# Optimization experiments

Hardware: AMD Instinct MI355X
Metric: run time of the kernel (lower is better)

The kernel has to match this reference:

```python
import jax, jax.numpy as jnp
import numpy as np

N = 50000   # nodes
E = 400000  # edges
IN_DIM, H1, H2, OUT_DIM = 512, 256, 62, 128


def _param(key, shape, scale=0.05):
    return jax.random.normal(key, shape, dtype=jnp.float32) * scale


def setup_inputs() -> dict:
    key = jax.random.key(0)
    ks = jax.random.split(key, 24)
    x = jax.random.normal(ks[0], (N, IN_DIM), dtype=jnp.float32)
    edge_index_neg = jax.random.randint(ks[1], (2, E), 0, N, dtype=jnp.int64)
    d = {
        "x": x, "edge_index_neg": edge_index_neg,
        # nn.Linear params (W stored as [in, out])
        "W1": _param(ks[2], (IN_DIM, H1)), "b1": _param(ks[3], (H1,)),
        "W2": _param(ks[4], (H1, H2)),    "b2": _param(ks[5], (H2,)),
        "W3": _param(ks[6], (H2, OUT_DIM)), "b3": _param(ks[7], (OUT_DIM,)),
        # GCNConv params: lin weight (no bias) + post-aggregation bias
        "Wg1": _param(ks[8], (H1, H1)),   "bg1": _param(ks[9], (H1,)),
        "Wg2": _param(ks[10], (H2, H2)),  "bg2": _param(ks[11], (H2,)),
        "Wg3": _param(ks[12], (OUT_DIM, OUT_DIM)), "bg3": _param(ks[13], (OUT_DIM,)),
        "Wg4": _param(ks[14], (OUT_DIM, OUT_DIM)), "bg4": _param(ks[15], (OUT_DIM,)),
        "Wg5": _param(ks[16], (OUT_DIM, OUT_DIM)), "bg5": _param(ks[17], (OUT_DIM,)),
        "Wg6": _param(ks[18], (OUT_DIM, OUT_DIM)), "bg6": _param(ks[19], (OUT_DIM,)),
    }
    return d


def _build_norm(edge_index):
    # PyG GCNConv: add self-loops, symmetric normalization D^-1/2 A D^-1/2
    loop = jnp.arange(N, dtype=edge_index.dtype)
    src = jnp.concatenate([edge_index[0], loop])
    dst = jnp.concatenate([edge_index[1], loop])
    deg = jax.ops.segment_sum(jnp.ones_like(dst, dtype=jnp.float32), dst, num_segments=N)
    dinv = jnp.where(deg > 0, jax.lax.rsqrt(jnp.maximum(deg, 1.0)), 0.0)
    norm = dinv[src] * dinv[dst]  # [E+N]
    return src, dst, norm


def _gcn(x, W, b, src, dst, norm):
    h = x @ W                                   # [N, F]
    msg = h[src] * norm[:, None]                # gather + edge scale
    out = jax.ops.segment_sum(msg, dst, num_segments=N)  # scatter-add
    return out + b


def reference(x, edge_index_neg, W1, b1, W2, b2, W3, b3,
              Wg1, bg1, Wg2, bg2, Wg3, bg3, Wg4, bg4, Wg5, bg5, Wg6, bg6):
    src, dst, norm = _build_norm(edge_index_neg)
    relu = jax.nn.relu
    x1l = x @ W1 + b1
    x1 = x1l + relu(_gcn(x1l, Wg1, bg1, src, dst, norm))
    x2l = x1 @ W2 + b2
    x2 = x2l + relu(_gcn(x2l, Wg2, bg2, src, dst, norm))
    x3l = x2 @ W3 + b3
    x3 = x3l + 0.5 * relu(_gcn(x3l, Wg3, bg3, src, dst, norm))
    x4 = x3 + 0.5 * relu(_gcn(x4_in := x3, Wg4, bg4, src, dst, norm))
    x5 = x4 + 0.25 * relu(_gcn(x4, Wg5, bg5, src, dst, norm))
    x6 = x5 + 0.25 * _gcn(x5, Wg6, bg6, src, dst, norm)
    return x6
```

## Files before the change

### kernel.cpp

```cpp
#include <hip/hip_runtime.h>

#define NN 50000
#define NE 400000
#define NBLK 196

using short8 = __attribute__((ext_vector_type(8))) short;
using f32x4  = __attribute__((ext_vector_type(4))) float;
using f32x2  = __attribute__((ext_vector_type(2))) float;
using u16x2  = __attribute__((ext_vector_type(2))) unsigned short;
using u16x4  = __attribute__((ext_vector_type(4))) unsigned short;

__device__ __forceinline__ unsigned short f2b(float f) {
    union { float f; unsigned int u; } x; x.f = f;
    unsigned int u = x.u;
    u += 0x7fffu + ((u >> 16) & 1u);
    return (unsigned short)(u >> 16);
}
__device__ __forceinline__ float b2f(unsigned short u) {
    union { unsigned int u; float f; } x; x.u = ((unsigned int)u) << 16;
    return x.f;
}

#define SWZ(b, row) ((b) ^ (((row) & 7) << 4))

__device__ __forceinline__ void gload16(const void* g, void* l) {
    __builtin_amdgcn_global_load_lds(
        (const __attribute__((address_space(1))) void*)g,
        (__attribute__((address_space(3))) void*)l, 16, 0, 0);
}

__global__ __launch_bounds__(256) void zero2_k(int* a, int* b) {
    int i = blockIdx.x * 256 + threadIdx.x;
    if (i < NN) { a[i] = 0; b[i] = 0; }
}
__global__ __launch_bounds__(256) void count_k(const int* __restrict__ dst, int* __restrict__ indeg) {
    int e = blockIdx.x * 256 + threadIdx.x;
    if (e < NE) atomicAdd(&indeg[dst[e]], 1);
}
__global__ __launch_bounds__(256) void scan1_k(const int* __restrict__ indeg, int* __restrict__ tmp,
                                               int* __restrict__ bsum) {
    __shared__ int s[256];
    int t = threadIdx.x, i = blockIdx.x * 256 + t;
    int v = (i < NN) ? indeg[i] : 0;
    s[t] = v; __syncthreads();
    for (int off = 1; off < 256; off <<= 1) {
        int x = (t >= off) ? s[t - off] : 0;
        __syncthreads();
        s[t] += x;
        __syncthreads();
    }
    if (i < NN) tmp[i] = s[t];
    if (t == 255) bsum[blockIdx.x] = s[255];
}
__global__ __launch_bounds__(256) void scan2_k(const int* __restrict__ bsum, int* __restrict__ boff) {
    __shared__ int s[256];
    int t = threadIdx.x;
    int v = (t < NBLK) ? bsum[t] : 0;
    s[t] = v; __syncthreads();
    for (int off = 1; off < 256; off <<= 1) {
        int x = (t >= off) ? s[t - off] : 0;
        __syncthreads();
        s[t] += x;
        __syncthreads();
    }
    if (t < NBLK) boff[t] = s[t] - v;
}
__global__ __launch_bounds__(256) void scan3_k(const int* __restrict__ tmp, const int* __restrict__ indeg,
                                               const int* __restrict__ boff, int* __restrict__ rowptr,
                                               float* __restrict__ dinv) {
    int i = blockIdx.x * 256 + threadIdx.x;
    if (i < NN) {
        rowptr[i] = tmp[i] - indeg[i] + boff[i >> 8];
        dinv[i] = rsqrtf((float)(1 + indeg[i]));
    }
    if (i == 0) rowptr[NN] = NE;
}
__global__ __launch_bounds__(256) void fill_k(const int* __restrict__ src, const int* __restrict__ dst,
                                              const float* __restrict__ dinv, const int* __restrict__ rowptr,
                                              int* __restrict__ cursor, int2* __restrict__ ebn) {
    int e = blockIdx.x * 256 + threadIdx.x;
    if (e >= NE) return;
    int s = src[e], d = dst[e];
    int pos = atomicAdd(&cursor[d], 1);
    ebn[rowptr[d] + pos] = make_int2(s, __float_as_int(dinv[s] * dinv[d]));
}

__global__ __launch_bounds__(256) void xcast_k(const float* __restrict__ x, unsigned short* __restrict__ xb) {
    long i = (long)blockIdx.x * 256 + threadIdx.x;
    const long total = (long)NN * 512 / 8;
    if (i >= total) return;
    float4 f0 = *(const float4*)(x + i * 8);
    float4 f1 = *(const float4*)(x + i * 8 + 4);
    short8 v;
    v[0] = (short)f2b(f0.x); v[1] = (short)f2b(f0.y);
    v[2] = (short)f2b(f0.z); v[3] = (short)f2b(f0.w);
    v[4] = (short)f2b(f1.x); v[5] = (short)f2b(f1.y);
    v[6] = (short)f2b(f1.z); v[7] = (short)f2b(f1.w);
    *(short8*)(xb + i * 8) = v;
}

struct WSegs {
    const float* W[9];
    unsigned short* Wt[9];
    int K[9], N[9], Kp[9];
    int c0[10];
};
__global__ __launch_bounds__(256) void wcast_all_k(WSegs s) {
    int blk = blockIdx.x;
    #pragma unroll
    for (int g = 0; g < 9; g++) {
        if (blk >= s.c0[g] && blk < s.c0[g + 1]) {
            int idx = (blk - s.c0[g]) * 256 + threadIdx.x;
            int Kp = s.Kp[g];
            int n = idx / Kp, k = idx % Kp;
            float v = (n < s.N[g] && k < s.K[g]) ? s.W[g][(size_t)k * s.N[g] + n] : 0.0f;
            s.Wt[g][idx] = f2b(v);
        }
    }
}

template<int BM, int BN>
__global__ __launch_bounds__(256) void gemm_mfma_k(
    const unsigned short* __restrict__ A, const unsigned short* __restrict__ Bt,
    const float* __restrict__ bias, unsigned short* __restrict__ C,
    int M, int lda, int Kp, int N, int ldc) {
    constexpr int MR = BM / 32;
    constexpr int NF = BN / 32;
    constexpr int nA = BM / 32;
    constexpr int nB = BN / 32;
    constexpr int BUFB = (BM + BN) * 128;
    __shared__ __align__(16) char lds[2 * BUFB];

    int tid = threadIdx.x;
    int lane = tid & 63, wave = tid >> 6;
    int wr = wave >> 1, wc = wave & 1;
    int lr = lane & 15, lk = lane >> 4;
    int r0 = blockIdx.x * BM, c0 = blockIdx.y * BN;

    f32x4 acc[MR][NF];
    #pragma unroll
    for (int m = 0; m < MR; m++)
        #pragma unroll
        for (int n = 0; n < NF; n++)
            acc[m][n] = (f32x4){0.f, 0.f, 0.f, 0.f};

    auto ISSUE = [&](int k0, char* buf) {
        char* AsB = buf;
        char* BsB = buf + BM * 128;
        #pragma unroll
        for (int c = 0; c < nA; c++) {
            int o = tid + c * 256;
            int row = o >> 3;
            int octg = (o & 7) ^ (row & 7);
            int gr = min(r0 + row, M - 1);
            gload16(A + (size_t)gr * lda + k0 + octg * 8, AsB + o * 16);
        }
        #pragma unroll
        for (int c = 0; c < nB; c++) {
            int o = tid + c * 256;
            int row = o >> 3;
            int octg = (o & 7) ^ (row & 7);
            gload16(Bt + (size_t)(c0 + row) * Kp + k0 + octg * 8, BsB + o * 16);
        }
    };

    int nt = Kp >> 6;
    ISSUE(0, lds);
    __syncthreads();
    for (int t = 0; t < nt; t++) {
        char* cur = lds + (t & 1) * BUFB;
        if (t + 1 < nt) ISSUE((t + 1) << 6, lds + ((t + 1) & 1) * BUFB);
        char* AsB = cur;
        char* BsB = cur + BM * 128;
        #pragma unroll
        for (int kk = 0; kk < 2; kk++) {
            int kb = kk * 64 + lk * 16;
            short8 a[MR], b[NF];
            #pragma unroll
            for (int m = 0; m < MR; m++) {
                int row = wr * (BM / 2) + m * 16 + lr;
                a[m] = *(short8*)(AsB + SWZ(row * 128 + kb, row));
            }
            #pragma unroll
            for (int n = 0; n < NF; n++) {
                int row = wc * (BN / 2) + n * 16 + lr;
                b[n] = *(short8*)(BsB + SWZ(row * 128 + kb, row));
            }
            #pragma unroll
            for (int m = 0; m < MR; m++)
                #pragma unroll
                for (int n = 0; n < NF; n++)
                    acc[m][n] = __builtin_amdgcn_mfma_f32_16x16x32_bf16(a[m], b[n], acc[m][n], 0, 0, 0);
        }
        __syncthreads();
    }

    constexpr int LDC = BN + 8;
    unsigned short* ldsC = (unsigned short*)lds;
    #pragma unroll
    for (int n = 0; n < NF; n++) {
        int cc = wc * (BN / 2) + n * 16 + lr;
        int gc = c0 + cc;
        float bv = (bias != nullptr && gc < N) ? bias[gc] : 0.0f;
        bool ok = gc < N;
        #pragma unroll
        for (int m = 0; m < MR; m++)
            #pragma unroll
            for (int j = 0; j < 4; j++) {
                int row = wr * (BM / 2) + m * 16 + lk * 4 + j;
                float v = ok ? acc[m][n][j] + bv : 0.0f;
                ldsC[row * LDC + cc] = f2b(v);
            }
    }
    __syncthreads();
    constexpr int CH = (BM * BN) / 2048;
    #pragma unroll
    for (int c = 0; c < CH; c++) {
        int o = tid + c * 256;
        int row = o / (BN / 8), col = (o % (BN / 8)) * 8;
        int gr = r0 + row;
        if (gr < M)
            *(short8*)(C + (size_t)gr * ldc + c0 + col) = *(short8*)(ldsC + row * LDC + col);
    }
}

template<int VEC> struct BV;
template<> struct BV<1> { using T = unsigned short; };
template<> struct BV<2> { using T = u16x2; };
template<> struct BV<4> { using T = u16x4; };
template<int VEC> struct FV;
template<> struct FV<1> { using T = float; };
template<> struct FV<2> { using T = f32x2; };
template<> struct FV<4> { using T = f32x4; };

template<int VEC, int SPLIT, bool OUTF32>
__global__ __launch_bounds__(256) void gather_k(
    const unsigned short* __restrict__ h, const unsigned short* __restrict__ base,
    const float* __restrict__ dinv, const float* __restrict__ bias,
    const int2* __restrict__ ebn, const int* __restrict__ rowptr,
    void* __restrict__ outraw, float alpha, int dorelu, int F) {
    constexpr int ld = 64 * VEC * SPLIT;
    int gw = (blockIdx.x * 256 + threadIdx.x) >> 6;
    int lane = threadIdx.x & 63;
    int w = gw / SPLIT;
    int colbase = (gw % SPLIT) * 64 * VEC;
    if (w >= NN) return;
    using LT = typename BV<VEC>::T;
    const int col = colbase + lane * VEC;

    float acc[VEC];
    float dn = dinv[w];
    {
        LT t = *(const LT*)(h + (size_t)w * ld + col);
        const unsigned short* tu = (const unsigned short*)&t;
        #pragma unroll
        for (int v = 0; v < VEC; v++) acc[v] = b2f(tu[v]) * dn * dn;
    }
    int e = rowptr[w], end = rowptr[w + 1];
    for (; e + 8 <= end; e += 8) {
        long long q[8];
        #pragma unroll
        for (int i = 0; i < 8; i++)
            q[i] = __builtin_nontemporal_load((const long long*)(ebn + e + i));
        LT t[8];
        #pragma unroll
        for (int i = 0; i < 8; i++)
            t[i] = *(const LT*)(h + (size_t)(int)q[i] * ld + col);
        #pragma unroll
        for (int i = 0; i < 8; i++) {
            float nr = __int_as_float((int)(q[i] >> 32));
            const unsigned short* u = (const unsigned short*)&t[i];
            #pragma unroll
            for (int v = 0; v < VEC; v++) acc[v] += b2f(u[v]) * nr;
        }
    }
    for (; e + 2 <= end; e += 2) {
        long long q0 = __builtin_nontemporal_load((const long long*)(ebn + e));
        long long q1 = __builtin_nontemporal_load((const long long*)(ebn + e + 1));
        LT t0 = *(const LT*)(h + (size_t)(int)q0 * ld + col);
        LT t1 = *(const LT*)(h + (size_t)(int)q1 * ld + col);
        float n0 = __int_as_float((int)(q0 >> 32)), n1 = __int_as_float((int)(q1 >> 32));
        const unsigned short* u0 = (const unsigned short*)&t0;
        const unsigned short* u1 = (const unsigned short*)&t1;
        #pragma unroll
        for (int v = 0; v < VEC; v++) acc[v] += b2f(u0[v]) * n0 + b2f(u1[v]) * n1;
    }
    if (e < end) {
        long long q0 = __builtin_nontemporal_load((const long long*)(ebn + e));
        LT t0 = *(const LT*)(h + (size_t)(int)q0 * ld + col);
        float n0 = __int_as_float((int)(q0 >> 32));
        const unsigned short* u0 = (const unsigned short*)&t0;
        #pragma unroll
        for (int v = 0; v < VEC; v++) acc[v] += b2f(u0[v]) * n0;
    }
    LT bt = __builtin_nontemporal_load((const LT*)(base + (size_t)w * ld + col));
    const unsigned short* bu = (const unsigned short*)&bt;
    if (OUTF32) {
        typename FV<VEC>::T ot;
        float* of = (float*)&ot;
        #pragma unroll
        for (int v = 0; v < VEC; v++) {
            int f = col + v;
            float a = acc[v] + ((f < F) ? bias[f] : 0.0f);
            if (dorelu) a = fmaxf(a, 0.0f);
            of[v] = (f < F) ? b2f(bu[v]) + alpha * a : 0.0f;
        }
        __builtin_nontemporal_store(ot, (typename FV<VEC>::T*)((float*)outraw + (size_t)w * ld + col));
    } else {
        LT ot;
        unsigned short* ou = (unsigned short*)&ot;
        #pragma unroll
        for (int v = 0; v < VEC; v++) {
            int f = col + v;
            float a = acc[v] + ((f < F) ? bias[f] : 0.0f);
            if (dorelu) a = fmaxf(a, 0.0f);
            float res = (f < F) ? b2f(bu[v]) + alpha * a : 0.0f;
            ou[v] = f2b(res);
        }
        __builtin_nontemporal_store(ot, (LT*)((unsigned short*)outraw + (size_t)w * ld + col));
    }
}

extern "C" void kernel_launch(void* const* d_in, const int* in_sizes, int n_in,
                              void* d_out, int out_size, void* d_ws, size_t ws_size,
                              hipStream_t stream) {
    const float* x   = (const float*)d_in[0];
    const int*   ei  = (const int*)d_in[1];
    const float* W1  = (const float*)d_in[2];  const float* b1  = (const float*)d_in[3];
    const float* W2  = (const float*)d_in[4];  const float* b2  = (const float*)d_in[5];
    const float* W3  = (const float*)d_in[6];  const float* b3  = (const float*)d_in[7];
    const float* Wg1 = (const float*)d_in[8];  const float* bg1 = (const float*)d_in[9];
    const float* Wg2 = (const float*)d_in[10]; const float* bg2 = (const float*)d_in[11];
    const float* Wg3 = (const float*)d_in[12]; const float* bg3 = (const float*)d_in[13];
    const float* Wg4 = (const float*)d_in[14]; const float* bg4 = (const float*)d_in[15];
    const float* Wg5 = (const float*)d_in[16]; const float* bg5 = (const float*)d_in[17];
    const float* Wg6 = (const float*)d_in[18]; const float* bg6 = (const float*)d_in[19];
    const int* srcv = ei;
    const int* dstv = ei + NE;

    float* dinv = (float*)d_ws;
    unsigned short* xb = (unsigned short*)(dinv + 51200);
    unsigned short* hA = xb + (size_t)NN * 512;
    unsigned short* hB = hA + (size_t)NN * 256;
    unsigned short* hC = hB + (size_t)NN * 256;
    unsigned short* W1t  = hC + (size_t)NN * 256;
    unsigned short* Wg1t = W1t  + 256 * 512;
    unsigned short* W2t  = Wg1t + 256 * 256;
    unsigned short* Wg2t = W2t  + 64 * 256;
    unsigned short* W3t  = Wg2t + 64 * 64;
    unsigned short* Wg3t = W3t  + 128 * 64;
    unsigned short* Wg4t = Wg3t + 128 * 128;
    unsigned short* Wg5t = Wg4t + 128 * 128;
    unsigned short* Wg6t = Wg5t + 128 * 128;
    int* indeg  = (int*)(Wg6t + 128 * 128);
    int* cursor = indeg + 51200;
    int* tmp    = cursor + 51200;
    int* rowptr = tmp + 51200;
    int* bsum   = rowptr + 51264;
    int* boff   = bsum + 256;
    int2* ebn   = (int2*)(boff + 256);

    zero2_k<<<NBLK, 256, 0, stream>>>(indeg, cursor);
    count_k<<<(NE + 255) / 256, 256, 0, stream>>>(dstv, indeg);
    scan1_k<<<NBLK, 256, 0, stream>>>(indeg, tmp, bsum);
    scan2_k<<<1, 256, 0, stream>>>(bsum, boff);
    scan3_k<<<NBLK, 256, 0, stream>>>(tmp, indeg, boff, rowptr, dinv);
    fill_k<<<(NE + 255) / 256, 256, 0, stream>>>(srcv, dstv, dinv, rowptr, cursor, ebn);

    xcast_k<<<(int)(((long)NN * 512 / 8 + 255) / 256), 256, 0, stream>>>(x, xb);

    {
        WSegs s;
        const float* Ws[9] = {W1, Wg1, W2, Wg2, W3, Wg3, Wg4, Wg5, Wg6};
        unsigned short* Wts[9] = {W1t, Wg1t, W2t, Wg2t, W3t, Wg3t, Wg4t, Wg5t, Wg6t};
        int Ks[9]  = {512, 256, 256, 62, 62, 128, 128, 128, 128};
        int Ns[9]  = {256, 256, 62, 62, 128, 128, 128, 128, 128};
        int Kps[9] = {512, 256, 256, 64, 64, 128, 128, 128, 128};
        int Nps[9] = {256, 256, 64, 64, 128, 128, 128, 128, 128};
        int c = 0;
        for (int g = 0; g < 9; g++) {
            s.W[g] = Ws[g]; s.Wt[g] = Wts[g];
            s.K[g] = Ks[g]; s.N[g] = Ns[g]; s.Kp[g] = Kps[g];
            s.c0[g] = c;
            c += (Kps[g] * Nps[g]) / 256;
        }
        s.c0[9] = c;
        wcast_all_k<<<c, 256, 0, stream>>>(s);
    }

    const int GX = (NN + 63) / 64;
    const int GG1 = (NN * 64 + 255) / 256;
    const int GG2 = (NN * 2 * 64 + 255) / 256;

    gemm_mfma_k<64, 128><<<dim3(GX, 2), 256, 0, stream>>>(xb, W1t, b1, hA, NN, 512, 512, 256, 256);
    gemm_mfma_k<64, 128><<<dim3(GX, 2), 256, 0, stream>>>(hA, Wg1t, nullptr, hB, NN, 256, 256, 256, 256);
    gather_k<2, 2, false><<<GG2, 256, 0, stream>>>(hB, hA, dinv, bg1, ebn, rowptr, hC, 1.0f, 1, 256);
    gemm_mfma_k<64, 64><<<dim3(GX, 1), 256, 0, stream>>>(hC, W2t, b2, hA, NN, 256, 256, 62, 64);
    gemm_mfma_k<64, 64><<<dim3(GX, 1), 256, 0, stream>>>(hA, Wg2t, nullptr, hB, NN, 64, 64, 62, 64);
    gather_k<1, 1, false><<<GG1, 256, 0, stream>>>(hB, hA, dinv, bg2, ebn, rowptr, hC, 1.0f, 1, 62);
    gemm_mfma_k<64, 64><<<dim3(GX, 2), 256, 0, stream>>>(hC, W3t, b3, hA, NN, 64, 64, 128, 128);
    gemm_mfma_k<64, 64><<<dim3(GX, 2), 256, 0, stream>>>(hA, Wg3t, nullptr, hB, NN, 128, 128, 128, 128);
    gather_k<2, 1, false><<<GG1, 256, 0, stream>>>(hB, hA, dinv, bg3, ebn, rowptr, hC, 0.5f, 1, 128);
    gemm_mfma_k<64, 64><<<dim3(GX, 2), 256, 0, stream>>>(hC, Wg4t, nullptr, hA, NN, 128, 128, 128, 128);
    gather_k<2, 1, false><<<GG1, 256, 0, stream>>>(hA, hC, dinv, bg4, ebn, rowptr, hB, 0.5f, 1, 128);
    gemm_mfma_k<64, 64><<<dim3(GX, 2), 256, 0, stream>>>(hB, Wg5t, nullptr, hA, NN, 128, 128, 128, 128);
    gather_k<2, 1, false><<<GG1, 256, 0, stream>>>(hA, hB, dinv, bg5, ebn, rowptr, hC, 0.25f, 1, 128);
    gemm_mfma_k<64, 64><<<dim3(GX, 2), 256, 0, stream>>>(hC, Wg6t, nullptr, hA, NN, 128, 128, 128, 128);
    gather_k<2, 1, true><<<GG1, 256, 0, stream>>>(hA, hC, dinv, bg6, ebn, rowptr, d_out, 0.25f, 0, 128);
}
```

Before: 407.6 us.

## Process two destination nodes per wave in gather and widen GEMM N tiles

```diff
diff --git a/kernel.cpp b/kernel.cpp
--- a/kernel.cpp
+++ b/kernel.cpp
@@ -240,84 +240,143 @@
     const int2* __restrict__ ebn, const int* __restrict__ rowptr,
     void* __restrict__ outraw, float alpha, int dorelu, int F) {
     constexpr int ld = 64 * VEC * SPLIT;
+    using LT = typename BV<VEC>::T;
     int gw = (blockIdx.x * 256 + threadIdx.x) >> 6;
     int lane = threadIdx.x & 63;
-    int w = gw / SPLIT;
-    int colbase = (gw % SPLIT) * 64 * VEC;
-    if (w >= NN) return;
-    using LT = typename BV<VEC>::T;
-    const int col = colbase + lane * VEC;
-
-    float acc[VEC];
-    float dn = dinv[w];
+    int pair = gw / SPLIT;
+    int colseg = gw % SPLIT;
+    int w0 = pair * 2, w1 = w0 + 1;
+    if (w0 >= NN) return;
+    bool has1 = (w1 < NN);
+    const int col = colseg * 64 * VEC + lane * VEC;
+
+    float acc0[VEC], acc1[VEC];
+    float dn0 = dinv[w0];
     {
-        LT t = *(const LT*)(h + (size_t)w * ld + col);
+        LT t = *(const LT*)(h + (size_t)w0 * ld + col);
         const unsigned short* tu = (const unsigned short*)&t;
         #pragma unroll
-        for (int v = 0; v < VEC; v++) acc[v] = b2f(tu[v]) * dn * dn;
-    }
-    int e = rowptr[w], end = rowptr[w + 1];
-    for (; e + 8 <= end; e += 8) {
-        long long q[8];
-        #pragma unroll
-        for (int i = 0; i < 8; i++)
-            q[i] = __builtin_nontemporal_load((const long long*)(ebn + e + i));
-        LT t[8];
-        #pragma unroll
-        for (int i = 0; i < 8; i++)
-            t[i] = *(const LT*)(h + (size_t)(int)q[i] * ld + col);
-        #pragma unroll
-        for (int i = 0; i < 8; i++) {
+        for (int v = 0; v < VEC; v++) acc0[v] = b2f(tu[v]) * dn0 * dn0;
+    }
+    if (has1) {
+        float dn1 = dinv[w1];
+        LT t = *(const LT*)(h + (size_t)w1 * ld + col);
+        const unsigned short* tu = (const unsigned short*)&t;
+        #pragma unroll
+        for (int v = 0; v < VEC; v++) acc1[v] = b2f(tu[v]) * dn1 * dn1;
+    } else {
+        #pragma unroll
+        for (int v = 0; v < VEC; v++) acc1[v] = 0.0f;
+    }
+
+    int e0 = rowptr[w0], end0 = rowptr[w0 + 1];
+    int e1 = has1 ? end0 : 0, end1 = has1 ? rowptr[w1 + 1] : 0;
+
+    while (e0 + 4 <= end0 && e1 + 4 <= end1) {
+        long long q0[4], q1[4];
+        #pragma unroll
+        for (int i = 0; i < 4; i++) {
+            q0[i] = __builtin_nontemporal_load((const long long*)(ebn + e0 + i));
+            q1[i] = __builtin_nontemporal_load((const long long*)(ebn + e1 + i));
+        }
+        LT t0[4], t1[4];
+        #pragma unroll
+        for (int i = 0; i < 4; i++) {
+            t0[i] = *(const LT*)(h + (size_t)(int)q0[i] * ld + col);
+            t1[i] = *(const LT*)(h + (size_t)(int)q1[i] * ld + col);
+        }
+        #pragma unroll
+        for (int i = 0; i < 4; i++) {
+            float n0 = __int_as_float((int)(q0[i] >> 32));
+            float n1 = __int_as_float((int)(q1[i] >> 32));
+            const unsigned short* u0 = (const unsigned short*)&t0[i];
+            const unsigned short* u1 = (const unsigned short*)&t1[i];
+            #pragma unroll
+            for (int v = 0; v < VEC; v++) {
+                acc0[v] += b2f(u0[v]) * n0;
+                acc1[v] += b2f(u1[v]) * n1;
+            }
+        }
+        e0 += 4; e1 += 4;
+    }
+    for (; e0 + 4 <= end0; e0 += 4) {
+        long long q[4];
+        #pragma unroll
+        for (int i = 0; i < 4; i++) q[i] = __builtin_nontemporal_load((const long long*)(ebn + e0 + i));
+        LT t[4];
+        #pragma unroll
+        for (int i = 0; i < 4; i++) t[i] = *(const LT*)(h + (size_t)(int)q[i] * ld + col);
+        #pragma unroll
+        for (int i = 0; i < 4; i++) {
             float nr = __int_as_float((int)(q[i] >> 32));
             const unsigned short* u = (const unsigned short*)&t[i];
             #pragma unroll
-            for (int v = 0; v < VEC; v++) acc[v] += b2f(u[v]) * nr;
-        }
-    }
-    for (; e + 2 <= end; e += 2) {
-        long long q0 = __builtin_nontemporal_load((const long long*)(ebn + e));
-        long long q1 = __builtin_nontemporal_load((const long long*)(ebn + e + 1));
-        LT t0 = *(const LT*)(h + (size_t)(int)q0 * ld + col);
-        LT t1 = *(const LT*)(h + (size_t)(int)q1 * ld + col);
-        float n0 = __int_as_float((int)(q0 >> 32)), n1 = __int_as_float((int)(q1 >> 32));
-        const unsigned short* u0 = (const unsigned short*)&t0;
-        const unsigned short* u1 = (const unsigned short*)&t1;
-        #pragma unroll
-        for (int v = 0; v < VEC; v++) acc[v] += b2f(u0[v]) * n0 + b2f(u1[v]) * n1;
-    }
-    if (e < end) {
-        long long q0 = __builtin_nontemporal_load((const long long*)(ebn + e));
-        LT t0 = *(const LT*)(h + (size_t)(int)q0 * ld + col);
-        float n0 = __int_as_float((int)(q0 >> 32));
-        const unsigned short* u0 = (const unsigned short*)&t0;
-        #pragma unroll
-        for (int v = 0; v < VEC; v++) acc[v] += b2f(u0[v]) * n0;
-    }
-    LT bt = __builtin_nontemporal_load((const LT*)(base + (size_t)w * ld + col));
-    const unsigned short* bu = (const unsigned short*)&bt;
-    if (OUTF32) {
-        typename FV<VEC>::T ot;
-        float* of = (float*)&ot;
-        #pragma unroll
-        for (int v = 0; v < VEC; v++) {
-            int f = col + v;
-            float a = acc[v] + ((f < F) ? bias[f] : 0.0f);
-            if (dorelu) a = fmaxf(a, 0.0f);
-            of[v] = (f < F) ? b2f(bu[v]) + alpha * a : 0.0f;
-        }
-        __builtin_nontemporal_store(ot, (typename FV<VEC>::T*)((float*)outraw + (size_t)w * ld + col));
-    } else {
-        LT ot;
-        unsigned short* ou = (unsigned short*)&ot;
-        #pragma unroll
-        for (int v = 0; v < VEC; v++) {
-            int f = col + v;
-            float a = acc[v] + ((f < F) ? bias[f] : 0.0f);
-            if (dorelu) a = fmaxf(a, 0.0f);
-            float res = (f < F) ? b2f(bu[v]) + alpha * a : 0.0f;
-            ou[v] = f2b(res);
-        }
-        __builtin_nontemporal_store(ot, (LT*)((unsigned short*)outraw + (size_t)w * ld + col));
+            for (int v = 0; v < VEC; v++) acc0[v] += b2f(u[v]) * nr;
+        }
+    }
+    for (; e0 < end0; e0++) {
+        long long q = __builtin_nontemporal_load((const long long*)(ebn + e0));
+        LT t = *(const LT*)(h + (size_t)(int)q * ld + col);
+        float nr = __int_as_float((int)(q >> 32));
+        const unsigned short* u = (const unsigned short*)&t;
+        #pragma unroll
+        for (int v = 0; v < VEC; v++) acc0[v] += b2f(u[v]) * nr;
+    }
+    for (; e1 + 4 <= end1; e1 += 4) {
+        long long q[4];
+        #pragma unroll
+        for (int i = 0; i < 4; i++) q[i] = __builtin_nontemporal_load((const long long*)(ebn + e1 + i));
+        LT t[4];
+        #pragma unroll
+        for (int i = 0; i < 4; i++) t[i] = *(const LT*)(h + (size_t)(int)q[i] * ld + col);
+        #pragma unroll
+        for (int i = 0; i < 4; i++) {
+            float nr = __int_as_float((int)(q[i] >> 32));
+            const unsigned short* u = (const unsigned short*)&t[i];
+            #pragma unroll
+            for (int v = 0; v < VEC; v++) acc1[v] += b2f(u[v]) * nr;
+        }
+    }
+    for (; e1 < end1; e1++) {
+        long long q = __builtin_nontemporal_load((const long long*)(ebn + e1));
+        LT t = *(const LT*)(h + (size_t)(int)q * ld + col);
+        float nr = __int_as_float((int)(q >> 32));
+        const unsigned short* u = (const unsigned short*)&t;
+        #pragma unroll
+        for (int v = 0; v < VEC; v++) acc1[v] += b2f(u[v]) * nr;
+    }
+
+    #pragma unroll
+    for (int nn = 0; nn < 2; nn++) {
+        int w = nn ? w1 : w0;
+        if (nn && !has1) break;
+        float* acc = nn ? acc1 : acc0;
+        LT bt = *(const LT*)(base + (size_t)w * ld + col);
+        const unsigned short* bu = (const unsigned short*)&bt;
+        if (OUTF32) {
+            typename FV<VEC>::T ot;
+            float* of = (float*)&ot;
+            #pragma unroll
+            for (int v = 0; v < VEC; v++) {
+                int f = col + v;
+                float a = acc[v] + ((f < F) ? bias[f] : 0.0f);
+                if (dorelu) a = fmaxf(a, 0.0f);
+                of[v] = (f < F) ? b2f(bu[v]) + alpha * a : 0.0f;
+            }
+            *(typename FV<VEC>::T*)((float*)outraw + (size_t)w * ld + col) = ot;
+        } else {
+            LT ot;
+            unsigned short* ou = (unsigned short*)&ot;
+            #pragma unroll
+            for (int v = 0; v < VEC; v++) {
+                int f = col + v;
+                float a = acc[v] + ((f < F) ? bias[f] : 0.0f);
+                if (dorelu) a = fmaxf(a, 0.0f);
+                float res = (f < F) ? b2f(bu[v]) + alpha * a : 0.0f;
+                ou[v] = f2b(res);
+            }
+            *(LT*)((unsigned short*)outraw + (size_t)w * ld + col) = ot;
+        }
     }
 }
 
@@ -389,22 +448,22 @@
     }
 
     const int GX = (NN + 63) / 64;
-    const int GG1 = (NN * 64 + 255) / 256;
-    const int GG2 = (NN * 2 * 64 + 255) / 256;
+    const int NPAIR = (NN + 1) / 2;
+    auto gwaves = [&](int split) { return (NPAIR * split * 64 + 255) / 256; };
 
     gemm_mfma_k<64, 128><<<dim3(GX, 2), 256, 0, stream>>>(xb, W1t, b1, hA, NN, 512, 512, 256, 256);
     gemm_mfma_k<64, 128><<<dim3(GX, 2), 256, 0, stream>>>(hA, Wg1t, nullptr, hB, NN, 256, 256, 256, 256);
-    gather_k<2, 2, false><<<GG2, 256, 0, stream>>>(hB, hA, dinv, bg1, ebn, rowptr, hC, 1.0f, 1, 256);
+    gather_k<4, 1, false><<<gwaves(1), 256, 0, stream>>>(hB, hA, dinv, bg1, ebn, rowptr, hC, 1.0f, 1, 256);
     gemm_mfma_k<64, 64><<<dim3(GX, 1), 256, 0, stream>>>(hC, W2t, b2, hA, NN, 256, 256, 62, 64);
     gemm_mfma_k<64, 64><<<dim3(GX, 1), 256, 0, stream>>>(hA, Wg2t, nullptr, hB, NN, 64, 64, 62, 64);
-    gather_k<1, 1, false><<<GG1, 256, 0, stream>>>(hB, hA, dinv, bg2, ebn, rowptr, hC, 1.0f, 1, 62);
-    gemm_mfma_k<64, 64><<<dim3(GX, 2), 256, 0, stream>>>(hC, W3t, b3, hA, NN, 64, 64, 128, 128);
-    gemm_mfma_k<64, 64><<<dim3(GX, 2), 256, 0, stream>>>(hA, Wg3t, nullptr, hB, NN, 128, 128, 128, 128);
-    gather_k<2, 1, false><<<GG1, 256, 0, stream>>>(hB, hA, dinv, bg3, ebn, rowptr, hC, 0.5f, 1, 128);
-    gemm_mfma_k<64, 64><<<dim3(GX, 2), 256, 0, stream>>>(hC, Wg4t, nullptr, hA, NN, 128, 128, 128, 128);
-    gather_k<2, 1, false><<<GG1, 256, 0, stream>>>(hA, hC, dinv, bg4, ebn, rowptr, hB, 0.5f, 1, 128);
-    gemm_mfma_k<64, 64><<<dim3(GX, 2), 256, 0, stream>>>(hB, Wg5t, nullptr, hA, NN, 128, 128, 128, 128);
-    gather_k<2, 1, false><<<GG1, 256, 0, stream>>>(hA, hB, dinv, bg5, ebn, rowptr, hC, 0.25f, 1, 128);
-    gemm_mfma_k<64, 64><<<dim3(GX, 2), 256, 0, stream>>>(hC, Wg6t, nullptr, hA, NN, 128, 128, 128, 128);
-    gather_k<2, 1, true><<<GG1, 256, 0, stream>>>(hA, hC, dinv, bg6, ebn, rowptr, d_out, 0.25f, 0, 128);
-}
+    gather_k<1, 1, false><<<gwaves(1), 256, 0, stream>>>(hB, hA, dinv, bg2, ebn, rowptr, hC, 1.0f, 1, 62);
+    gemm_mfma_k<64, 128><<<dim3(GX, 1), 256, 0, stream>>>(hC, W3t, b3, hA, NN, 64, 64, 128, 128);
+    gemm_mfma_k<64, 128><<<dim3(GX, 1), 256, 0, stream>>>(hA, Wg3t, nullptr, hB, NN, 128, 128, 128, 128);
+    gather_k<2, 1, false><<<gwaves(1), 256, 0, stream>>>(hB, hA, dinv, bg3, ebn, rowptr, hC, 0.5f, 1, 128);
+    gemm_mfma_k<64, 128><<<dim3(GX, 1), 256, 0, stream>>>(hC, Wg4t, nullptr, hA, NN, 128, 128, 128, 128);
+    gather_k<2, 1, false><<<gwaves(1), 256, 0, stream>>>(hA, hC, dinv, bg4, ebn, rowptr, hB, 0.5f, 1, 128);
+    gemm_mfma_k<64, 128><<<dim3(GX, 1), 256, 0, stream>>>(hB, Wg5t, nullptr, hA, NN, 128, 128, 128, 128);
+    gather_k<2, 1, false><<<gwaves(1), 256, 0, stream>>>(hA, hB, dinv, bg5, ebn, rowptr, hC, 0.25f, 1, 128);
+    gemm_mfma_k<64, 128><<<dim3(GX, 1), 256, 0, stream>>>(hC, Wg6t, nullptr, hA, NN, 128, 128, 128, 128);
+    gather_k<2, 1, true><<<gwaves(1), 256, 0, stream>>>(hA, hC, dinv, bg6, ebn, rowptr, d_out, 0.25f, 0, 128);
+}
```

After: 404.9 us. About the same (-0.7%).
